# Kernel tuning notes

Measured on AMD Instinct MI355X. Metric: run time of the kernel, lower is better.

The kernel has to match this reference:

```python
import jax, jax.numpy as jnp
import numpy as np

DX = DY = DZ = 128
C = 16
SIGMA = 0.5
TAU = 2.0
N = DX * DY * DZ


def _flat_grid():
    # [N, 3] float32 voxel coordinates, meshgrid 'ij' order
    gx, gy, gz = jnp.meshgrid(jnp.arange(DX, dtype=jnp.float32),
                              jnp.arange(DY, dtype=jnp.float32),
                              jnp.arange(DZ, dtype=jnp.float32), indexing='ij')
    return jnp.stack([gx, gy, gz], axis=-1).reshape(-1, 3)


def setup_inputs() -> dict:
    key = jax.random.key(0)
    k1, k2, k3 = jax.random.split(key, 3)
    B = 64
    ray_origin = jax.random.uniform(k1, (B, 3), dtype=jnp.float32) * 127.0
    d = jax.random.normal(k2, (B, 3), dtype=jnp.float32)
    ray_dir = d / jnp.linalg.norm(d, axis=-1, keepdims=True)
    memory = jax.random.normal(k3, (DX, DY, DZ, C), dtype=jnp.float32) * 0.01
    return {"ray_origin": ray_origin, "ray_dir": ray_dir, "memory": memory}


def reference(ray_origin, ray_dir, memory):
    # read(): per-ray Gaussian-tube kernel over the full grid, reduced against memory.
    grid = _flat_grid()                              # [N, 3]
    mem = memory.reshape(-1, C)                      # [N, C]
    g2 = jnp.sum(grid * grid, axis=-1)               # [N]
    o2 = jnp.sum(ray_origin * ray_origin, axis=-1)   # [B]
    d2 = jnp.sum(ray_dir * ray_dir, axis=-1)         # [B] (=1 for unit dirs)
    od = jnp.sum(ray_origin * ray_dir, axis=-1)      # [B]
    # t[b,n] = (grid[n]-origin[b]) . dir[b]
    t = jnp.einsum('nd,bd->bn', grid, ray_dir) - od[:, None]          # [B, N]
    # |dx|^2 = |grid|^2 - 2 grid.origin + |origin|^2
    dx2 = g2[None, :] - 2.0 * jnp.einsum('nd,bd->bn', grid, ray_origin) + o2[:, None]
    # r2 = |dx - t*dir|^2 = |dx|^2 - 2 t (dx.dir) + t^2 |dir|^2, with dx.dir = t
    r2 = dx2 - 2.0 * t * t + (t * t) * d2[:, None]
    kern = jnp.exp(-r2 / (2.0 * SIGMA ** 2) - jnp.abs(t) / TAU)        # [B, N]
    return jnp.einsum('bn,nc->bc', kern, mem)                          # [B, C]
```

## Files before the change

### kernel.cpp

```cpp
#include <hip/hip_runtime.h>
#include <math.h>

#define GD 128
#define NC 16
#define CUT 10.0f

__global__ __launch_bounds__(1024) void tube_read_kernel(
    const float* __restrict__ ro, const float* __restrict__ rd,
    const float* __restrict__ mem, float* __restrict__ out)
{
    const int b    = blockIdx.x;
    const int wave = threadIdx.x >> 6;
    const int lane = threadIdx.x & 63;

    const float ox = ro[b * 3 + 0], oy = ro[b * 3 + 1], oz = ro[b * 3 + 2];
    const float dx = rd[b * 3 + 0], dy = rd[b * 3 + 1], dz = rd[b * 3 + 2];
    const float d2 = dx * dx + dy * dy + dz * dz;
    const float c2 = 2.0f - d2;

    const float adx = fabsf(dx), ady = fabsf(dy), adz = fabsf(dz);

    float oa, da, ou, du, ov, dv;
    int sa, su, sv;
    if (adx >= ady && adx >= adz) {
        oa = ox; da = dx; ou = oy; du = dy; ov = oz; dv = dz;
        sa = GD * GD; su = GD; sv = 1;
    } else if (ady >= adz) {
        oa = oy; da = dy; ou = ox; du = dx; ov = oz; dv = dz;
        sa = GD; su = GD * GD; sv = 1;
    } else {
        oa = oz; da = dz; ou = ox; du = dx; ov = oy; dv = dy;
        sa = 1; su = GD * GD; sv = GD;
    }
    const float ada    = fabsf(da);
    const float inv_da = 1.0f / da;
    const float aida   = fabsf(inv_da);

    const float TMAX = 2.0f * CUT;
    const float RMAX = 2.35f;
    const float krange = TMAX * ada + RMAX + 0.5f;
    int kmin = (int)ceilf(oa - krange);  if (kmin < 0) kmin = 0;
    int kmax = (int)floorf(oa + krange); if (kmax > GD - 1) kmax = GD - 1;

    const float Ru = RMAX * (1.0f + fabsf(du) * aida) + 0.05f;
    const float Rv = RMAX * (1.0f + fabsf(dv) * aida) + 0.05f;

    float acc[NC];
#pragma unroll
    for (int c = 0; c < NC; ++c) acc[c] = 0.0f;

    const int lr = lane >> 3;
    const int lc = lane & 7;

    for (int k = kmin + wave; k <= kmax; k += 16) {
        const float fa = (float)k - oa;
        const float s  = fa * inv_da;
        const float qu = ou + s * du;
        const float qv = ov + s * dv;
        int u0 = (int)ceilf(qu - Ru);  if (u0 < 0) u0 = 0;
        int u1 = (int)floorf(qu + Ru); if (u1 > GD - 1) u1 = GD - 1;
        int v0 = (int)ceilf(qv - Rv);  if (v0 < 0) v0 = 0;
        int v1 = (int)floorf(qv + Rv); if (v1 > GD - 1) v1 = GD - 1;
        if (u1 < u0 || v1 < v0) continue;

        const int base_a = k * sa;
        for (int tu = u0 + lr; tu <= u1; tu += 8) {
            const float fu  = (float)tu - ou;
            const int  bu   = base_a + tu * su;
            for (int tv = v0 + lc; tv <= v1; tv += 8) {
                const float fv = (float)tv - ov;
                const float t  = fa * da + fu * du + fv * dv;
                const float q2 = fa * fa + fu * fu + fv * fv;
                const float r2 = q2 - t * t * c2;
                const float arg = -2.0f * r2 - 0.5f * fabsf(t);
                if (arg > -CUT) {
                    const float kern = __expf(arg);
                    const float4* m =
                        (const float4*)(mem + (size_t)(bu + tv * sv) * NC);
                    const float4 m0 = m[0], m1 = m[1], m2 = m[2], m3 = m[3];
                    acc[0]  += kern * m0.x; acc[1]  += kern * m0.y;
                    acc[2]  += kern * m0.z; acc[3]  += kern * m0.w;
                    acc[4]  += kern * m1.x; acc[5]  += kern * m1.y;
                    acc[6]  += kern * m1.z; acc[7]  += kern * m1.w;
                    acc[8]  += kern * m2.x; acc[9]  += kern * m2.y;
                    acc[10] += kern * m2.z; acc[11] += kern * m2.w;
                    acc[12] += kern * m3.x; acc[13] += kern * m3.y;
                    acc[14] += kern * m3.z; acc[15] += kern * m3.w;
                }
            }
        }
    }

    __shared__ float red[16 * NC];
#pragma unroll
    for (int c = 0; c < NC; ++c) {
        float v = acc[c];
        for (int off = 32; off; off >>= 1) v += __shfl_down(v, off);
        if (lane == 0) red[wave * NC + c] = v;
    }
    __syncthreads();
    if (threadIdx.x < NC) {
        float s = 0.0f;
#pragma unroll
        for (int w = 0; w < 16; ++w) s += red[w * NC + threadIdx.x];
        out[b * NC + threadIdx.x] = s;
    }
}

extern "C" void kernel_launch(void* const* d_in, const int* in_sizes, int n_in,
                              void* d_out, int out_size, void* d_ws, size_t ws_size,
                              hipStream_t stream) {
    const float* ray_origin = (const float*)d_in[0];
    const float* ray_dir    = (const float*)d_in[1];
    const float* memory     = (const float*)d_in[2];
    float* out = (float*)d_out;

    tube_read_kernel<<<dim3(64), dim3(1024), 0, stream>>>(
        ray_origin, ray_dir, memory, out);
}
```

Before: 12.76 us.

## Tighten tube cutoff, hoist partial dot products, use transpose-style wave reduction

New measurement: 13.07 us, median of 2. +2.4%, slower.

```diff
diff --git a/kernel.cpp b/kernel.cpp
--- a/kernel.cpp
+++ b/kernel.cpp
@@ -3,7 +3,7 @@
 
 #define GD 128
 #define NC 16
-#define CUT 10.0f
+#define CUT 8.0f
 
 __global__ __launch_bounds__(1024) void tube_read_kernel(
     const float* __restrict__ ro, const float* __restrict__ rd,
@@ -37,7 +37,7 @@
     const float aida   = fabsf(inv_da);
 
     const float TMAX = 2.0f * CUT;
-    const float RMAX = 2.35f;
+    const float RMAX = 2.05f;
     const float krange = TMAX * ada + RMAX + 0.5f;
     int kmin = (int)ceilf(oa - krange);  if (kmin < 0) kmin = 0;
     int kmax = (int)floorf(oa + krange); if (kmax > GD - 1) kmax = GD - 1;
@@ -63,14 +63,18 @@
         int v1 = (int)floorf(qv + Rv); if (v1 > GD - 1) v1 = GD - 1;
         if (u1 < u0 || v1 < v0) continue;
 
+        const float ta = fa * da;
+        const float qa = fa * fa;
         const int base_a = k * sa;
         for (int tu = u0 + lr; tu <= u1; tu += 8) {
             const float fu  = (float)tu - ou;
+            const float tb  = ta + fu * du;
+            const float qb  = qa + fu * fu;
             const int  bu   = base_a + tu * su;
             for (int tv = v0 + lc; tv <= v1; tv += 8) {
                 const float fv = (float)tv - ov;
-                const float t  = fa * da + fu * du + fv * dv;
-                const float q2 = fa * fa + fu * fu + fv * fv;
+                const float t  = tb + fv * dv;
+                const float q2 = qb + fv * fv;
                 const float r2 = q2 - t * t * c2;
                 const float arg = -2.0f * r2 - 0.5f * fabsf(t);
                 if (arg > -CUT) {
@@ -91,19 +95,44 @@
         }
     }
 
-    __shared__ float red[16 * NC];
+    float v8[8];
 #pragma unroll
-    for (int c = 0; c < NC; ++c) {
-        float v = acc[c];
-        for (int off = 32; off; off >>= 1) v += __shfl_down(v, off);
-        if (lane == 0) red[wave * NC + c] = v;
+    for (int j = 0; j < 8; ++j) {
+        const float send = (lane & 1) ? acc[j]     : acc[j + 8];
+        const float keep = (lane & 1) ? acc[j + 8] : acc[j];
+        v8[j] = keep + __shfl_xor(send, 1);
     }
-    __syncthreads();
-    if (threadIdx.x < NC) {
-        float s = 0.0f;
+    float v4[4];
 #pragma unroll
-        for (int w = 0; w < 16; ++w) s += red[w * NC + threadIdx.x];
-        out[b * NC + threadIdx.x] = s;
+    for (int j = 0; j < 4; ++j) {
+        const float send = (lane & 2) ? v8[j]     : v8[j + 4];
+        const float keep = (lane & 2) ? v8[j + 4] : v8[j];
+        v4[j] = keep + __shfl_xor(send, 2);
+    }
+    float v2[2];
+#pragma unroll
+    for (int j = 0; j < 2; ++j) {
+        const float send = (lane & 4) ? v4[j]     : v4[j + 2];
+        const float keep = (lane & 4) ? v4[j + 2] : v4[j];
+        v2[j] = keep + __shfl_xor(send, 4);
+    }
+    {
+        const float send = (lane & 8) ? v2[0] : v2[1];
+        const float keep = (lane & 8) ? v2[1] : v2[0];
+        float v1 = keep + __shfl_xor(send, 8);
+        v1 += __shfl_xor(v1, 16);
+        v1 += __shfl_xor(v1, 32);
+        const int c = ((lane & 1) << 3) | ((lane & 2) << 1)
+                    | ((lane & 4) >> 1) | ((lane & 8) >> 3);
+        __shared__ float red[16 * NC];
+        if (lane < 16) red[wave * NC + c] = v1;
+        __syncthreads();
+        if (threadIdx.x < NC) {
+            float ssum = 0.0f;
+#pragma unroll
+            for (int w = 0; w < 16; ++w) ssum += red[w * NC + threadIdx.x];
+            out[b * NC + threadIdx.x] = ssum;
+        }
     }
 }
 
```
